# Kernel optimization log

Hardware: AMD Instinct MI355X
Metric: run time of the kernel (lower is better)

## Reference

```python
import jax, jax.numpy as jnp
import numpy as np

B, L, E, R, A = 1024, 40, 1024, 1024, 512


def setup_inputs() -> dict:
    key = jax.random.key(0)
    ks = jax.random.split(key, 20)
    s = 0.05  # weight scale to avoid gate saturation
    inp = {
        "xt": jax.random.normal(ks[0], (B, E), jnp.float32),
        "xt_mask": jnp.ones((B, 1), jnp.float32),
        "V": jax.random.normal(ks[1], (B, L, R), jnp.float32),
        "pos_feat": jax.random.normal(ks[2], (B, R), jnp.float32),
        "h1": jax.random.normal(ks[3], (1, B, R), jnp.float32),
        "c1": jax.random.normal(ks[4], (1, B, R), jnp.float32),
        "h2": jax.random.normal(ks[5], (1, B, R), jnp.float32),
        "c2": jax.random.normal(ks[6], (1, B, R), jnp.float32),
        "Wg": jax.random.normal(ks[7], (E, R), jnp.float32) * s,
        "bg": jnp.zeros((R,), jnp.float32),
        "Wi1": jax.random.normal(ks[8], (E, 4 * R), jnp.float32) * s,
        "bi1": jnp.zeros((4 * R,), jnp.float32),
        "Wa1": jax.random.normal(ks[9], (R, 4 * R), jnp.float32) * s,
        "ba1": jnp.zeros((4 * R,), jnp.float32),
        "Wh1": jax.random.normal(ks[10], (R, 4 * R), jnp.float32) * s,
        "bh1": jnp.zeros((4 * R,), jnp.float32),
        "Wi2": jax.random.normal(ks[11], (R, 4 * R), jnp.float32) * s,
        "bi2": jnp.zeros((4 * R,), jnp.float32),
        "Wa2": jax.random.normal(ks[12], (R, 4 * R), jnp.float32) * s,
        "ba2": jnp.zeros((4 * R,), jnp.float32),
        "Wh2": jax.random.normal(ks[13], (R, 4 * R), jnp.float32) * s,
        "bh2": jnp.zeros((4 * R,), jnp.float32),
        "Wv2a": jax.random.normal(ks[14], (R, A), jnp.float32) * s,
        "bv2a": jnp.zeros((A,), jnp.float32),
        "Wh2a": jax.random.normal(ks[15], (2 * R, A), jnp.float32) * s,
        "bh2a": jnp.zeros((A,), jnp.float32),
        "Wa2w": jax.random.normal(ks[16], (A, 1), jnp.float32) * s,
        "ba2w": jnp.zeros((1,), jnp.float32),
    }
    return inp


def _lstm_cell(in1, in2, h, c, Wi, bi, Wa, ba, Wh, bh, mask):
    # all_input_sums: [B, 4R]; torch gate order: i, f, o (sigmoid) then g (tanh)
    s = in1 @ Wi + bi + in2 @ Wa + ba + h @ Wh + bh
    i_g = jax.nn.sigmoid(s[:, 0 * R:1 * R])
    f_g = jax.nn.sigmoid(s[:, 1 * R:2 * R])
    o_g = jax.nn.sigmoid(s[:, 2 * R:3 * R])
    g = jnp.tanh(s[:, 3 * R:4 * R])
    c_new = f_g * c + i_g * g
    c_new = c_new * mask + c * (1.0 - mask)
    h_new = o_g * jnp.tanh(c_new)
    h_new = h_new * mask + h * (1.0 - mask)
    return h_new, c_new


def reference(xt, xt_mask, V, pos_feat, h1, c1, h2, c2,
              Wg, bg, Wi1, bi1, Wa1, ba1, Wh1, bh1,
              Wi2, bi2, Wa2, ba2, Wh2, bh2,
              Wv2a, bv2a, Wh2a, bh2a, Wa2w, ba2w):
    h1l, c1l = h1[-1], c1[-1]  # [B, R]
    h2l, c2l = h2[-1], c2[-1]
    # additive attention over L frames
    hq = jnp.concatenate([h1l, h2l], axis=1) @ Wh2a + bh2a        # [B, A]
    e = jnp.tanh(hq[:, None, :] + V @ Wv2a + bv2a) @ Wa2w + ba2w  # [B, L, 1]
    w = jax.nn.softmax(e, axis=1)                                  # softmax over L
    af = jnp.sum(w * V, axis=1)                                    # [B, R]
    # gate (dropout in eval mode -> identity)
    gate = jax.nn.relu(xt @ Wg + bg)
    gated_pos = gate * pos_feat + pos_feat
    # two-layer LSTM
    out1, c1n = _lstm_cell(xt, gated_pos, h1l, c1l, Wi1, bi1, Wa1, ba1, Wh1, bh1, xt_mask)
    out2, c2n = _lstm_cell(out1, af, h2l, c2l, Wi2, bi2, Wa2, ba2, Wh2, bh2, xt_mask)
    return (out2, out1[None], c1n[None], out2[None], c2n[None])
```

## Files before the change

kernel.cpp:

```cpp
#include <hip/hip_runtime.h>
#include <math.h>

#define BB 1024
#define LL 40
#define RR 1024

using short8 = __attribute__((ext_vector_type(8))) short;
using us8    = __attribute__((ext_vector_type(8))) unsigned short;
using f32x4  = __attribute__((ext_vector_type(4))) float;

__device__ __forceinline__ ushort f2bf(float f) {
    union { float f; unsigned u; } a; a.f = f;
    unsigned r = a.u + 0x7fffu + ((a.u >> 16) & 1u);
    return (ushort)(r >> 16);
}
__device__ __forceinline__ float bf2f(ushort u) {
    union { unsigned u; float f; } a; a.u = ((unsigned)u) << 16;
    return a.f;
}
__device__ __forceinline__ float ftanh(float x) {
    float cx = fminf(fmaxf(x, -15.f), 15.f);
    float e = __expf(2.f * cx);
    return (e - 1.f) / (e + 1.f);
}
__device__ __forceinline__ float fsigmoid(float x) {
    float cx = fminf(fmaxf(x, -30.f), 30.f);
    return 1.f / (1.f + __expf(-cx));
}

__device__ __forceinline__ void gll16(const ushort* g, ushort* l) {
    __builtin_amdgcn_global_load_lds(
        (const __attribute__((address_space(1))) void*)g,
        (__attribute__((address_space(3))) void*)l,
        16, 0, 0);
}

__global__ __launch_bounds__(256) void conv_bf16_kernel(
    const float* __restrict__ src, ushort* __restrict__ dst, int n8)
{
    const int i = blockIdx.x * 256 + threadIdx.x;
    if (i >= n8) return;
    const float4* s4 = (const float4*)(src + (size_t)i * 8);
    float4 x = s4[0], y = s4[1];
    us8 v;
    v[0] = f2bf(x.x); v[1] = f2bf(x.y); v[2] = f2bf(x.z); v[3] = f2bf(x.w);
    v[4] = f2bf(y.x); v[5] = f2bf(y.y); v[6] = f2bf(y.z); v[7] = f2bf(y.w);
    ((us8*)dst)[i] = v;
}

struct CP3 { const float* in[3]; ushort* out[3]; };
__global__ __launch_bounds__(256) void conv_bf16_batch3_kernel(CP3 p, int n8)
{
    const int z = blockIdx.y;
    const int i = blockIdx.x * 256 + threadIdx.x;
    if (i >= n8) return;
    const float4* s4 = (const float4*)(p.in[z] + (size_t)i * 8);
    float4 x = s4[0], y = s4[1];
    us8 v;
    v[0] = f2bf(x.x); v[1] = f2bf(x.y); v[2] = f2bf(x.z); v[3] = f2bf(x.w);
    v[4] = f2bf(y.x); v[5] = f2bf(y.y); v[6] = f2bf(y.z); v[7] = f2bf(y.w);
    ((us8*)p.out[z])[i] = v;
}

struct TP6 { const float* in[6]; ushort* out[6]; int N[6]; };
__global__ __launch_bounds__(256) void transpose_conv_kernel(TP6 p)
{
    const int z = blockIdx.z;
    const int Nn = p.N[z];
    const int n0 = blockIdx.x * 64;
    if (n0 >= Nn) return;
    const int k0 = blockIdx.y * 64;
    const float* in = p.in[z];
    ushort* out = p.out[z];

    __shared__ float tile[64][65];
    const int t = threadIdx.x;
    const int tx = t & 63, ty = t >> 6;
#pragma unroll
    for (int r = 0; r < 16; ++r) {
        const int row = ty * 16 + r;
        tile[row][tx] = in[(size_t)(k0 + row) * Nn + n0 + tx];
    }
    __syncthreads();
    const int n = t >> 2, kq = t & 3;
    us8 v0, v1;
#pragma unroll
    for (int j = 0; j < 8; ++j) v0[j] = f2bf(tile[kq * 16 + j][n]);
#pragma unroll
    for (int j = 0; j < 8; ++j) v1[j] = f2bf(tile[kq * 16 + 8 + j][n]);
    ushort* op = out + (size_t)(n0 + n) * 1024 + k0 + kq * 16;
    *(us8*)op = v0;
    *((us8*)op + 1) = v1;
}

template <int NP, int SK, int EPI>
__global__ __launch_bounds__(256) void gemm_gl(
    const ushort* __restrict__ A0, const ushort* __restrict__ A1, const ushort* __restrict__ A2,
    const ushort* __restrict__ W0, const ushort* __restrict__ W1, const ushort* __restrict__ W2,
    float* __restrict__ C, int M, int N,
    const float* __restrict__ hq, const float* __restrict__ bv2a,
    const float* __restrict__ Wa2w, float* __restrict__ epart)
{
    __shared__ ushort As[128 * 32];
    __shared__ ushort Bs[128 * 32];

    const int t = threadIdx.x, lane = t & 63, wave = t >> 6;
    const int wm = wave >> 1, wn = wave & 1;

    int bx, by;
    if constexpr (EPI == 2) {
        const int lin = blockIdx.y * gridDim.x + blockIdx.x;
        const int swz = (lin & 7) * 160 + (lin >> 3);
        bx = swz & 3; by = swz >> 2;
    } else { bx = blockIdx.x; by = blockIdx.y; }
    const int m0 = by * 128, n0 = bx * 128;

    const int srow = 16 * wave + (lane >> 2);
    const int skq  = lane & 3;

    f32x4 acc[4][4];
#pragma unroll
    for (int i = 0; i < 4; ++i)
#pragma unroll
        for (int j = 0; j < 4; ++j) acc[i][j] = (f32x4){0.f, 0.f, 0.f, 0.f};

    const int total = NP * 32;
    const int per   = total / SK;
    const int s0v   = blockIdx.z * per;
    const int sEnd  = s0v + per;

    for (int s = s0v; s < sEnd; ++s) {
        const int p  = (NP == 1) ? 0 : (s >> 5);
        const int k0 = (s & 31) << 5;
        const ushort* Ap = (p == 0) ? A0 : ((p == 1) ? A1 : A2);
        const ushort* Wp = (p == 0) ? W0 : ((p == 1) ? W1 : W2);
        const ushort* ga = Ap + (size_t)(m0 + srow) * 1024 + k0 + skq * 8;
        const ushort* gb = Wp + (size_t)(n0 + srow) * 1024 + k0 + skq * 8;
        gll16(ga,                 &As[512 * wave]);
        gll16(ga + 64 * 1024,     &As[2048 + 512 * wave]);
        gll16(gb,                 &Bs[512 * wave]);
        gll16(gb + 64 * 1024,     &Bs[2048 + 512 * wave]);
        __syncthreads();

        short8 aF[4], bF[4];
#pragma unroll
        for (int mi = 0; mi < 4; ++mi)
            aF[mi] = *(const short8*)&As[(wm * 64 + mi * 16 + (lane & 15)) * 32 + (lane >> 4) * 8];
#pragma unroll
        for (int ni = 0; ni < 4; ++ni)
            bF[ni] = *(const short8*)&Bs[(wn * 64 + ni * 16 + (lane & 15)) * 32 + (lane >> 4) * 8];
#pragma unroll
        for (int mi = 0; mi < 4; ++mi)
#pragma unroll
            for (int ni = 0; ni < 4; ++ni)
                acc[mi][ni] = __builtin_amdgcn_mfma_f32_16x16x32_bf16(aF[mi], bF[ni], acc[mi][ni], 0, 0, 0);
        __syncthreads();
    }

    if constexpr (EPI == 3) {
        float* Cz = C + (size_t)blockIdx.z * M * N;
#pragma unroll
        for (int ni = 0; ni < 4; ++ni) {
            const int col = n0 + wn * 64 + ni * 16 + (lane & 15);
#pragma unroll
            for (int mi = 0; mi < 4; ++mi) {
                const int row = m0 + wm * 64 + mi * 16 + ((lane >> 4) << 2);
#pragma unroll
                for (int r = 0; r < 4; ++r)
                    Cz[(size_t)(row + r) * N + col] = acc[mi][ni][r];
            }
        }
    } else if constexpr (EPI == 2) {
        float* red = (float*)As;
        float wa[4], bv[4];
        int coln[4];
#pragma unroll
        for (int ni = 0; ni < 4; ++ni) {
            coln[ni] = n0 + wn * 64 + ni * 16 + (lane & 15);
            wa[ni] = Wa2w[coln[ni]];
            bv[ni] = bv2a[coln[ni]];
        }
#pragma unroll
        for (int mi = 0; mi < 4; ++mi) {
            const int rowl = wm * 64 + mi * 16 + ((lane >> 4) << 2);
#pragma unroll
            for (int r = 0; r < 4; ++r) {
                const int row = m0 + rowl + r;
                const int b = row / LL;
                float v = 0.f;
#pragma unroll
                for (int ni = 0; ni < 4; ++ni) {
                    float x = acc[mi][ni][r] + hq[(size_t)b * 512 + coln[ni]] + bv[ni];
                    v += ftanh(x) * wa[ni];
                }
                v += __shfl_xor(v, 1);
                v += __shfl_xor(v, 2);
                v += __shfl_xor(v, 4);
                v += __shfl_xor(v, 8);
                if ((lane & 15) == 0) red[(rowl + r) * 2 + wn] = v;
            }
        }
        __syncthreads();
        if (t < 128)
            epart[(size_t)(m0 + t) * 4 + bx] = red[t * 2] + red[t * 2 + 1];
    }
}

__global__ __launch_bounds__(256) void reduce_hq_kernel(
    const float* __restrict__ part, const float* __restrict__ bias, float* __restrict__ hq)
{
    const int i = blockIdx.x * 256 + threadIdx.x;
    float s = bias[i & 511];
#pragma unroll
    for (int z = 0; z < 8; ++z) s += part[(size_t)z * 524288 + i];
    hq[i] = s;
}

__global__ __launch_bounds__(256) void reduce_gate_kernel(
    const float* __restrict__ part, const float* __restrict__ bias,
    const float* __restrict__ pos, ushort* __restrict__ gpb)
{
    const int i = blockIdx.x * 256 + threadIdx.x;
    float s = bias[i & 1023];
#pragma unroll
    for (int z = 0; z < 4; ++z) s += part[(size_t)z * 1048576 + i];
    const float g = fmaxf(s, 0.f);
    gpb[i] = f2bf(g * pos[i] + pos[i]);
}

__global__ __launch_bounds__(256) void softmax_af_kernel(
    const float* __restrict__ epart, const ushort* __restrict__ Vb,
    const float* __restrict__ ba2w, ushort* __restrict__ afb)
{
    const int b = blockIdx.x;
    const int tid = threadIdx.x;
    __shared__ float e_raw[LL];
    __shared__ float e_exp[LL];

    if (tid < LL) {
        const float* ep = &epart[(size_t)(b * LL + tid) * 4];
        float e = ba2w[0];
#pragma unroll
        for (int c = 0; c < 4; ++c) e += ep[c];
        e_raw[tid] = e;
    }
    __syncthreads();
    float mx = -1e30f;
#pragma unroll
    for (int l = 0; l < LL; ++l) mx = fmaxf(mx, e_raw[l]);
    if (tid < LL) e_exp[tid] = __expf(e_raw[tid] - mx);
    __syncthreads();
    float sum = 0.f;
#pragma unroll
    for (int l = 0; l < LL; ++l) sum += e_exp[l];
    const float inv = 1.f / sum;

    const int r4 = tid * 4;
    const ushort* vp = &Vb[(size_t)b * LL * RR + r4];
    float a0 = 0.f, a1 = 0.f, a2 = 0.f, a3 = 0.f;
#pragma unroll 8
    for (int l = 0; l < LL; ++l) {
        ushort4 v = *(const ushort4*)&vp[(size_t)l * RR];
        const float w = e_exp[l];
        a0 += w * bf2f(v.x); a1 += w * bf2f(v.y);
        a2 += w * bf2f(v.z); a3 += w * bf2f(v.w);
    }
    ushort* op = &afb[(size_t)b * RR + r4];
    op[0] = f2bf(a0 * inv); op[1] = f2bf(a1 * inv);
    op[2] = f2bf(a2 * inv); op[3] = f2bf(a3 * inv);
}

__global__ __launch_bounds__(256) void lstm_finish4_kernel(
    const float* __restrict__ part,
    const float* __restrict__ bi, const float* __restrict__ ba, const float* __restrict__ bh,
    const float* __restrict__ c_in, const float* __restrict__ h_in, const float* __restrict__ mask,
    float* __restrict__ h_out, float* __restrict__ h_out2,
    float* __restrict__ c_out, ushort* __restrict__ h_bf)
{
    const int i = blockIdx.x * 256 + threadIdx.x;
    const int b = i >> 10;
    const int r = i & 1023;
    float sg[4];
#pragma unroll
    for (int g = 0; g < 4; ++g) {
        const int gr = g * 1024 + r;
        float s = bi[gr] + ba[gr] + bh[gr];
#pragma unroll
        for (int z = 0; z < 4; ++z)
            s += part[(size_t)z * 4194304 + (size_t)b * 4096 + gr];
        sg[g] = s;
    }
    const float ig = fsigmoid(sg[0]);
    const float fg = fsigmoid(sg[1]);
    const float og = fsigmoid(sg[2]);
    const float gt = ftanh(sg[3]);
    const float m = mask[b];
    const float c = c_in[i];
    float cn = fg * c + ig * gt;
    cn = cn * m + c * (1.f - m);
    const float h = h_in[i];
    float hn = og * ftanh(cn);
    hn = hn * m + h * (1.f - m);
    h_out[i] = hn;
    if (h_out2) h_out2[i] = hn;
    c_out[i] = cn;
    if (h_bf) h_bf[i] = f2bf(hn);
}

extern "C" void kernel_launch(void* const* d_in, const int* in_sizes, int n_in,
                              void* d_out, int out_size, void* d_ws, size_t ws_size,
                              hipStream_t stream) {
    const float* xt   = (const float*)d_in[0];
    const float* mask = (const float*)d_in[1];
    const float* V    = (const float*)d_in[2];
    const float* pos  = (const float*)d_in[3];
    const float* h1   = (const float*)d_in[4];
    const float* c1   = (const float*)d_in[5];
    const float* h2   = (const float*)d_in[6];
    const float* c2   = (const float*)d_in[7];
    const float* Wg   = (const float*)d_in[8];
    const float* bg   = (const float*)d_in[9];
    const float* Wi1  = (const float*)d_in[10];
    const float* bi1  = (const float*)d_in[11];
    const float* Wa1  = (const float*)d_in[12];
    const float* ba1  = (const float*)d_in[13];
    const float* Wh1  = (const float*)d_in[14];
    const float* bh1  = (const float*)d_in[15];
    const float* Wi2  = (const float*)d_in[16];
    const float* bi2  = (const float*)d_in[17];
    const float* Wa2  = (const float*)d_in[18];
    const float* ba2  = (const float*)d_in[19];
    const float* Wh2  = (const float*)d_in[20];
    const float* bh2  = (const float*)d_in[21];
    const float* Wv2a = (const float*)d_in[22];
    const float* bv2a = (const float*)d_in[23];
    const float* Wh2a = (const float*)d_in[24];
    const float* bh2a = (const float*)d_in[25];
    const float* Wa2w = (const float*)d_in[26];
    const float* ba2w = (const float*)d_in[27];

    float* out = (float*)d_out;
    float* out2  = out;
    float* out1  = out + (size_t)BB * RR;
    float* c1n   = out + 2 * (size_t)BB * RR;
    float* out2b = out + 3 * (size_t)BB * RR;
    float* c2n   = out + 4 * (size_t)BB * RR;

    ushort* wsu = (ushort*)d_ws;
    size_t o = 0;
    ushort* Vb     = wsu + o; o += (size_t)40960 * 1024;
    ushort* Wh2aT0 = wsu + o; o += (size_t)512 * 1024;
    ushort* Wh2aT1 = wsu + o; o += (size_t)512 * 1024;
    ushort* WgT    = wsu + o; o += (size_t)1024 * 1024;
    ushort* Wv2aT  = wsu + o; o += (size_t)512 * 1024;
    ushort* Wi1T   = wsu + o; o += (size_t)4096 * 1024;
    ushort* Wa1T   = wsu + o; o += (size_t)4096 * 1024;
    ushort* Wh1T   = wsu + o; o += (size_t)4096 * 1024;
    ushort* Wi2T   = wsu + o; o += (size_t)4096 * 1024;
    ushort* Wa2T   = wsu + o; o += (size_t)4096 * 1024;
    ushort* Wh2T   = wsu + o; o += (size_t)4096 * 1024;
    ushort* xtb    = wsu + o; o += (size_t)1024 * 1024;
    ushort* h1b    = wsu + o; o += (size_t)1024 * 1024;
    ushort* h2b    = wsu + o; o += (size_t)1024 * 1024;
    ushort* gpb    = wsu + o; o += (size_t)1024 * 1024;
    ushort* afb    = wsu + o; o += (size_t)1024 * 1024;
    ushort* out1b  = wsu + o; o += (size_t)1024 * 1024;
    float* wsf    = (float*)(wsu + o);
    float* hqf    = wsf;
    float* epart  = hqf + 524288;
    float* partSm = epart + 163840;
    float* partK  = (float*)Vb;

    const dim3 blk(256);

    conv_bf16_kernel<<<dim3(20480), blk, 0, stream>>>(V, Vb, 5242880);
    {
        CP3 p; p.in[0] = xt; p.in[1] = h1; p.in[2] = h2;
        p.out[0] = xtb; p.out[1] = h1b; p.out[2] = h2b;
        conv_bf16_batch3_kernel<<<dim3(512, 3), blk, 0, stream>>>(p, 131072);
    }
    {
        TP6 p;
        p.in[0] = Wi1; p.in[1] = Wa1; p.in[2] = Wh1;
        p.in[3] = Wi2; p.in[4] = Wa2; p.in[5] = Wh2;
        p.out[0] = Wi1T; p.out[1] = Wa1T; p.out[2] = Wh1T;
        p.out[3] = Wi2T; p.out[4] = Wa2T; p.out[5] = Wh2T;
        for (int z = 0; z < 6; ++z) p.N[z] = 4096;
        transpose_conv_kernel<<<dim3(64, 16, 6), blk, 0, stream>>>(p);
    }
    {
        TP6 p;
        p.in[0] = Wh2a; p.in[1] = Wh2a + (size_t)1024 * 512;
        p.in[2] = Wg;   p.in[3] = Wv2a;
        p.out[0] = Wh2aT0; p.out[1] = Wh2aT1; p.out[2] = WgT; p.out[3] = Wv2aT;
        p.N[0] = 512; p.N[1] = 512; p.N[2] = 1024; p.N[3] = 512;
        p.in[4] = nullptr; p.in[5] = nullptr; p.out[4] = nullptr; p.out[5] = nullptr;
        p.N[4] = 0; p.N[5] = 0;
        transpose_conv_kernel<<<dim3(16, 16, 4), blk, 0, stream>>>(p);
    }

    gemm_gl<2, 8, 3><<<dim3(4, 8, 8), blk, 0, stream>>>(
        h1b, h2b, nullptr, Wh2aT0, Wh2aT1, nullptr,
        partSm, 1024, 512, nullptr, nullptr, nullptr, nullptr);
    reduce_hq_kernel<<<dim3(2048), blk, 0, stream>>>(partSm, bh2a, hqf);

    gemm_gl<1, 4, 3><<<dim3(8, 8, 4), blk, 0, stream>>>(
        xtb, nullptr, nullptr, WgT, nullptr, nullptr,
        partSm, 1024, 1024, nullptr, nullptr, nullptr, nullptr);
    reduce_gate_kernel<<<dim3(4096), blk, 0, stream>>>(partSm, bg, pos, gpb);

    gemm_gl<1, 1, 2><<<dim3(4, 320, 1), blk, 0, stream>>>(
        Vb, nullptr, nullptr, Wv2aT, nullptr, nullptr,
        nullptr, 40960, 512, hqf, bv2a, Wa2w, epart);
    softmax_af_kernel<<<dim3(BB), blk, 0, stream>>>(epart, Vb, ba2w, afb);

    gemm_gl<3, 4, 3><<<dim3(32, 8, 4), blk, 0, stream>>>(
        xtb, gpb, h1b, Wi1T, Wa1T, Wh1T,
        partK, 1024, 4096, nullptr, nullptr, nullptr, nullptr);
    lstm_finish4_kernel<<<dim3(4096), blk, 0, stream>>>(
        partK, bi1, ba1, bh1, c1, h1, mask, out1, nullptr, c1n, out1b);

    gemm_gl<3, 4, 3><<<dim3(32, 8, 4), blk, 0, stream>>>(
        out1b, afb, h2b, Wi2T, Wa2T, Wh2T,
        partK, 1024, 4096, nullptr, nullptr, nullptr, nullptr);
    lstm_finish4_kernel<<<dim3(4096), blk, 0, stream>>>(
        partK, bi2, ba2, bh2, c2, h2, mask, out2, out2b, c2n, nullptr);
}
```

Baseline: 329.0 us.

## Replace GEMM with 256x256 double-buffered 512-thread kernel and bf16 split-K partials

```diff
diff --git a/kernel.cpp b/kernel.cpp
--- a/kernel.cpp
+++ b/kernel.cpp
@@ -93,96 +93,144 @@
     *((us8*)op + 1) = v1;
 }
 
-template <int NP, int SK, int EPI>
-__global__ __launch_bounds__(256) void gemm_gl(
+template <int NP, int NTZ, int EPI>
+__global__ __launch_bounds__(512) void gemm256(
     const ushort* __restrict__ A0, const ushort* __restrict__ A1, const ushort* __restrict__ A2,
     const ushort* __restrict__ W0, const ushort* __restrict__ W1, const ushort* __restrict__ W2,
-    float* __restrict__ C, int M, int N,
+    ushort* __restrict__ Cp, int M, int N,
     const float* __restrict__ hq, const float* __restrict__ bv2a,
     const float* __restrict__ Wa2w, float* __restrict__ epart)
 {
-    __shared__ ushort As[128 * 32];
-    __shared__ ushort Bs[128 * 32];
-
-    const int t = threadIdx.x, lane = t & 63, wave = t >> 6;
-    const int wm = wave >> 1, wn = wave & 1;
-
-    int bx, by;
+    __shared__ ushort As[2][256 * 64];
+    __shared__ ushort Bs[2][256 * 64];
+
+    const int t = threadIdx.x, l = t & 63, w = t >> 6;
+    const int wm = w >> 2, wn = w & 3;
+
+    int mblk, nblk, bz;
     if constexpr (EPI == 2) {
-        const int lin = blockIdx.y * gridDim.x + blockIdx.x;
-        const int swz = (lin & 7) * 160 + (lin >> 3);
-        bx = swz & 3; by = swz >> 2;
-    } else { bx = blockIdx.x; by = blockIdx.y; }
-    const int m0 = by * 128, n0 = bx * 128;
-
-    const int srow = 16 * wave + (lane >> 2);
-    const int skq  = lane & 3;
-
-    f32x4 acc[4][4];
-#pragma unroll
-    for (int i = 0; i < 4; ++i)
+        const int lin = blockIdx.x;
+        const int swz = (lin & 7) * 40 + (lin >> 3);
+        nblk = swz & 1; mblk = swz >> 1; bz = 0;
+    } else {
+        const int Dx = gridDim.x, Dy = gridDim.y;
+        const int lin = blockIdx.x + blockIdx.y * Dx + blockIdx.z * Dx * gridDim.y;
+        const int nwg = Dx * Dy * gridDim.z;
+        const int cpx = nwg >> 3;
+        const int swz = (lin & 7) * cpx + (lin >> 3);
+        mblk = swz % Dx;
+        const int rest = swz / Dx;
+        nblk = rest % Dy;
+        bz = rest / Dy;
+    }
+    const int m0 = mblk * 256, n0 = nblk * 256;
+
+    f32x4 acc[8][4];
+#pragma unroll
+    for (int i = 0; i < 8; ++i)
 #pragma unroll
         for (int j = 0; j < 4; ++j) acc[i][j] = (f32x4){0.f, 0.f, 0.f, 0.f};
 
-    const int total = NP * 32;
-    const int per   = total / SK;
-    const int s0v   = blockIdx.z * per;
-    const int sEnd  = s0v + per;
-
-    for (int s = s0v; s < sEnd; ++s) {
-        const int p  = (NP == 1) ? 0 : (s >> 5);
-        const int k0 = (s & 31) << 5;
+    const int rsub = w * 8 + (l >> 3);
+    const int csw  = ((l & 7) ^ (l >> 3)) * 8;
+
+    const int kx0 = ((0 * 4 + (l >> 4)) ^ (l & 7)) * 8;
+    const int kx1 = ((1 * 4 + (l >> 4)) ^ (l & 7)) * 8;
+
+    const int gt0 = bz * NTZ;
+
+    auto stage = [&](int s, int buf) {
+        const int p  = (NP == 1) ? 0 : (s >> 4);
+        const int k0 = (s & 15) << 6;
         const ushort* Ap = (p == 0) ? A0 : ((p == 1) ? A1 : A2);
         const ushort* Wp = (p == 0) ? W0 : ((p == 1) ? W1 : W2);
-        const ushort* ga = Ap + (size_t)(m0 + srow) * 1024 + k0 + skq * 8;
-        const ushort* gb = Wp + (size_t)(n0 + srow) * 1024 + k0 + skq * 8;
-        gll16(ga,                 &As[512 * wave]);
-        gll16(ga + 64 * 1024,     &As[2048 + 512 * wave]);
-        gll16(gb,                 &Bs[512 * wave]);
-        gll16(gb + 64 * 1024,     &Bs[2048 + 512 * wave]);
-        __syncthreads();
-
-        short8 aF[4], bF[4];
-#pragma unroll
-        for (int mi = 0; mi < 4; ++mi)
-            aF[mi] = *(const short8*)&As[(wm * 64 + mi * 16 + (lane & 15)) * 32 + (lane >> 4) * 8];
-#pragma unroll
-        for (int ni = 0; ni < 4; ++ni)
-            bF[ni] = *(const short8*)&Bs[(wn * 64 + ni * 16 + (lane & 15)) * 32 + (lane >> 4) * 8];
-#pragma unroll
-        for (int mi = 0; mi < 4; ++mi)
-#pragma unroll
-            for (int ni = 0; ni < 4; ++ni)
-                acc[mi][ni] = __builtin_amdgcn_mfma_f32_16x16x32_bf16(aF[mi], bF[ni], acc[mi][ni], 0, 0, 0);
-        __syncthreads();
+#pragma unroll
+        for (int j = 0; j < 4; ++j) {
+            gll16(Ap + (size_t)(m0 + j * 64 + rsub) * 1024 + k0 + csw,
+                  &As[buf][(j * 64 + w * 8) * 64]);
+            gll16(Wp + (size_t)(n0 + j * 64 + rsub) * 1024 + k0 + csw,
+                  &Bs[buf][(j * 64 + w * 8) * 64]);
+        }
+    };
+
+    stage(gt0, 0);
+    stage(gt0 + 1, 1);
+    asm volatile("s_waitcnt vmcnt(8)" ::: "memory");
+    __builtin_amdgcn_s_barrier();
+    asm volatile("" ::: "memory");
+
+    int cur = 0;
+    for (int ti = 0; ti < NTZ; ++ti) {
+#pragma unroll
+        for (int qm = 0; qm < 2; ++qm) {
+            short8 aF[4][2];
+#pragma unroll
+            for (int mi = 0; mi < 4; ++mi) {
+                const int ro = (wm * 128 + (qm * 4 + mi) * 16 + (l & 15)) * 64;
+                aF[mi][0] = *(const short8*)&As[cur][ro + kx0];
+                aF[mi][1] = *(const short8*)&As[cur][ro + kx1];
+            }
+#pragma unroll
+            for (int qn = 0; qn < 2; ++qn) {
+                short8 bF[2][2];
+#pragma unroll
+                for (int ni = 0; ni < 2; ++ni) {
+                    const int ro = (wn * 64 + (qn * 2 + ni) * 16 + (l & 15)) * 64;
+                    bF[ni][0] = *(const short8*)&Bs[cur][ro + kx0];
+                    bF[ni][1] = *(const short8*)&Bs[cur][ro + kx1];
+                }
+                __builtin_amdgcn_s_setprio(1);
+#pragma unroll
+                for (int mi = 0; mi < 4; ++mi)
+#pragma unroll
+                    for (int ni = 0; ni < 2; ++ni) {
+                        acc[qm * 4 + mi][qn * 2 + ni] = __builtin_amdgcn_mfma_f32_16x16x32_bf16(
+                            aF[mi][0], bF[ni][0], acc[qm * 4 + mi][qn * 2 + ni], 0, 0, 0);
+                        acc[qm * 4 + mi][qn * 2 + ni] = __builtin_amdgcn_mfma_f32_16x16x32_bf16(
+                            aF[mi][1], bF[ni][1], acc[qm * 4 + mi][qn * 2 + ni], 0, 0, 0);
+                    }
+                __builtin_amdgcn_s_setprio(0);
+            }
+        }
+        asm volatile("" ::: "memory");
+        __builtin_amdgcn_s_barrier();
+        asm volatile("" ::: "memory");
+        if (ti + 2 < NTZ) stage(gt0 + ti + 2, cur);
+        if (ti + 1 < NTZ) {
+            if (ti + 2 < NTZ) asm volatile("s_waitcnt vmcnt(8)" ::: "memory");
+            else              asm volatile("s_waitcnt vmcnt(0)" ::: "memory");
+            __builtin_amdgcn_s_barrier();
+            asm volatile("" ::: "memory");
+        }
+        cur ^= 1;
     }
 
     if constexpr (EPI == 3) {
-        float* Cz = C + (size_t)blockIdx.z * M * N;
+        ushort* Cz = Cp + (size_t)bz * M * N;
 #pragma unroll
         for (int ni = 0; ni < 4; ++ni) {
-            const int col = n0 + wn * 64 + ni * 16 + (lane & 15);
-#pragma unroll
-            for (int mi = 0; mi < 4; ++mi) {
-                const int row = m0 + wm * 64 + mi * 16 + ((lane >> 4) << 2);
+            const int col = n0 + wn * 64 + ni * 16 + (l & 15);
+#pragma unroll
+            for (int mi = 0; mi < 8; ++mi) {
+                const int row = m0 + wm * 128 + mi * 16 + ((l >> 4) << 2);
 #pragma unroll
                 for (int r = 0; r < 4; ++r)
-                    Cz[(size_t)(row + r) * N + col] = acc[mi][ni][r];
+                    Cz[(size_t)(row + r) * N + col] = f2bf(acc[mi][ni][r]);
             }
         }
     } else if constexpr (EPI == 2) {
-        float* red = (float*)As;
+        float* red = (float*)&As[0][0];
         float wa[4], bv[4];
         int coln[4];
 #pragma unroll
         for (int ni = 0; ni < 4; ++ni) {
-            coln[ni] = n0 + wn * 64 + ni * 16 + (lane & 15);
+            coln[ni] = n0 + wn * 64 + ni * 16 + (l & 15);
             wa[ni] = Wa2w[coln[ni]];
             bv[ni] = bv2a[coln[ni]];
         }
 #pragma unroll
-        for (int mi = 0; mi < 4; ++mi) {
-            const int rowl = wm * 64 + mi * 16 + ((lane >> 4) << 2);
+        for (int mi = 0; mi < 8; ++mi) {
+            const int rowl = wm * 128 + mi * 16 + ((l >> 4) << 2);
 #pragma unroll
             for (int r = 0; r < 4; ++r) {
                 const int row = m0 + rowl + r;
@@ -197,33 +245,35 @@
                 v += __shfl_xor(v, 2);
                 v += __shfl_xor(v, 4);
                 v += __shfl_xor(v, 8);
-                if ((lane & 15) == 0) red[(rowl + r) * 2 + wn] = v;
+                if ((l & 15) == 0) red[(rowl + r) * 4 + wn] = v;
             }
         }
         __syncthreads();
-        if (t < 128)
-            epart[(size_t)(m0 + t) * 4 + bx] = red[t * 2] + red[t * 2 + 1];
-    }
-}
-
-__global__ __launch_bounds__(256) void reduce_hq_kernel(
-    const float* __restrict__ part, const float* __restrict__ bias, float* __restrict__ hq)
+        if (t < 256) {
+            float s = red[t * 4] + red[t * 4 + 1] + red[t * 4 + 2] + red[t * 4 + 3];
+            epart[(size_t)(m0 + t) * 2 + nblk] = s;
+        }
+    }
+}
+
+__global__ __launch_bounds__(256) void reduce_hq_b_kernel(
+    const ushort* __restrict__ part, const float* __restrict__ bias, float* __restrict__ hq)
 {
     const int i = blockIdx.x * 256 + threadIdx.x;
     float s = bias[i & 511];
 #pragma unroll
-    for (int z = 0; z < 8; ++z) s += part[(size_t)z * 524288 + i];
+    for (int z = 0; z < 8; ++z) s += bf2f(part[(size_t)z * 524288 + i]);
     hq[i] = s;
 }
 
-__global__ __launch_bounds__(256) void reduce_gate_kernel(
-    const float* __restrict__ part, const float* __restrict__ bias,
+__global__ __launch_bounds__(256) void reduce_gate_b_kernel(
+    const ushort* __restrict__ part, const float* __restrict__ bias,
     const float* __restrict__ pos, ushort* __restrict__ gpb)
 {
     const int i = blockIdx.x * 256 + threadIdx.x;
     float s = bias[i & 1023];
 #pragma unroll
-    for (int z = 0; z < 4; ++z) s += part[(size_t)z * 1048576 + i];
+    for (int z = 0; z < 4; ++z) s += bf2f(part[(size_t)z * 1048576 + i]);
     const float g = fmaxf(s, 0.f);
     gpb[i] = f2bf(g * pos[i] + pos[i]);
 }
@@ -238,40 +288,37 @@
     __shared__ float e_exp[LL];
 
     if (tid < LL) {
-        const float* ep = &epart[(size_t)(b * LL + tid) * 4];
-        float e = ba2w[0];
-#pragma unroll
-        for (int c = 0; c < 4; ++c) e += ep[c];
-        e_raw[tid] = e;
+        const float* ep = &epart[(size_t)(b * LL + tid) * 2];
+        e_raw[tid] = ba2w[0] + ep[0] + ep[1];
     }
     __syncthreads();
     float mx = -1e30f;
 #pragma unroll
-    for (int l = 0; l < LL; ++l) mx = fmaxf(mx, e_raw[l]);
+    for (int ll = 0; ll < LL; ++ll) mx = fmaxf(mx, e_raw[ll]);
     if (tid < LL) e_exp[tid] = __expf(e_raw[tid] - mx);
     __syncthreads();
     float sum = 0.f;
 #pragma unroll
-    for (int l = 0; l < LL; ++l) sum += e_exp[l];
+    for (int ll = 0; ll < LL; ++ll) sum += e_exp[ll];
     const float inv = 1.f / sum;
 
     const int r4 = tid * 4;
     const ushort* vp = &Vb[(size_t)b * LL * RR + r4];
     float a0 = 0.f, a1 = 0.f, a2 = 0.f, a3 = 0.f;
 #pragma unroll 8
-    for (int l = 0; l < LL; ++l) {
-        ushort4 v = *(const ushort4*)&vp[(size_t)l * RR];
-        const float w = e_exp[l];
-        a0 += w * bf2f(v.x); a1 += w * bf2f(v.y);
-        a2 += w * bf2f(v.z); a3 += w * bf2f(v.w);
+    for (int ll = 0; ll < LL; ++ll) {
+        ushort4 v = *(const ushort4*)&vp[(size_t)ll * RR];
+        const float wgt = e_exp[ll];
+        a0 += wgt * bf2f(v.x); a1 += wgt * bf2f(v.y);
+        a2 += wgt * bf2f(v.z); a3 += wgt * bf2f(v.w);
     }
     ushort* op = &afb[(size_t)b * RR + r4];
     op[0] = f2bf(a0 * inv); op[1] = f2bf(a1 * inv);
     op[2] = f2bf(a2 * inv); op[3] = f2bf(a3 * inv);
 }
 
-__global__ __launch_bounds__(256) void lstm_finish4_kernel(
-    const float* __restrict__ part,
+__global__ __launch_bounds__(256) void lstm_finishb_kernel(
+    const ushort* __restrict__ part,
     const float* __restrict__ bi, const float* __restrict__ ba, const float* __restrict__ bh,
     const float* __restrict__ c_in, const float* __restrict__ h_in, const float* __restrict__ mask,
     float* __restrict__ h_out, float* __restrict__ h_out2,
@@ -287,7 +334,7 @@
         float s = bi[gr] + ba[gr] + bh[gr];
 #pragma unroll
         for (int z = 0; z < 4; ++z)
-            s += part[(size_t)z * 4194304 + (size_t)b * 4096 + gr];
+            s += bf2f(part[(size_t)z * 4194304 + (size_t)b * 4096 + gr]);
         sg[g] = s;
     }
     const float ig = fsigmoid(sg[0]);
@@ -365,13 +412,14 @@
     ushort* gpb    = wsu + o; o += (size_t)1024 * 1024;
     ushort* afb    = wsu + o; o += (size_t)1024 * 1024;
     ushort* out1b  = wsu + o; o += (size_t)1024 * 1024;
+    ushort* partSb = wsu + o; o += (size_t)8 * 1024 * 512;
     float* wsf    = (float*)(wsu + o);
     float* hqf    = wsf;
     float* epart  = hqf + 524288;
-    float* partSm = epart + 163840;
-    float* partK  = (float*)Vb;
+    ushort* partKb = Vb;
 
     const dim3 blk(256);
+    const dim3 blk5(512);
 
     conv_bf16_kernel<<<dim3(20480), blk, 0, stream>>>(V, Vb, 5242880);
     {
@@ -399,30 +447,30 @@
         transpose_conv_kernel<<<dim3(16, 16, 4), blk, 0, stream>>>(p);
     }
 
-    gemm_gl<2, 8, 3><<<dim3(4, 8, 8), blk, 0, stream>>>(
+    gemm256<2, 4, 3><<<dim3(4, 2, 8), blk5, 0, stream>>>(
         h1b, h2b, nullptr, Wh2aT0, Wh2aT1, nullptr,
-        partSm, 1024, 512, nullptr, nullptr, nullptr, nullptr);
-    reduce_hq_kernel<<<dim3(2048), blk, 0, stream>>>(partSm, bh2a, hqf);
-
-    gemm_gl<1, 4, 3><<<dim3(8, 8, 4), blk, 0, stream>>>(
+        partSb, 1024, 512, nullptr, nullptr, nullptr, nullptr);
+    reduce_hq_b_kernel<<<dim3(2048), blk, 0, stream>>>(partSb, bh2a, hqf);
+
+    gemm256<1, 4, 3><<<dim3(4, 4, 4), blk5, 0, stream>>>(
         xtb, nullptr, nullptr, WgT, nullptr, nullptr,
-        partSm, 1024, 1024, nullptr, nullptr, nullptr, nullptr);
-    reduce_gate_kernel<<<dim3(4096), blk, 0, stream>>>(partSm, bg, pos, gpb);
-
-    gemm_gl<1, 1, 2><<<dim3(4, 320, 1), blk, 0, stream>>>(
+        partSb, 1024, 1024, nullptr, nullptr, nullptr, nullptr);
+    reduce_gate_b_kernel<<<dim3(4096), blk, 0, stream>>>(partSb, bg, pos, gpb);
+
+    gemm256<1, 16, 2><<<dim3(320), blk5, 0, stream>>>(
         Vb, nullptr, nullptr, Wv2aT, nullptr, nullptr,
         nullptr, 40960, 512, hqf, bv2a, Wa2w, epart);
     softmax_af_kernel<<<dim3(BB), blk, 0, stream>>>(epart, Vb, ba2w, afb);
 
-    gemm_gl<3, 4, 3><<<dim3(32, 8, 4), blk, 0, stream>>>(
+    gemm256<3, 12, 3><<<dim3(4, 16, 4), blk5, 0, stream>>>(
         xtb, gpb, h1b, Wi1T, Wa1T, Wh1T,
-        partK, 1024, 4096, nullptr, nullptr, nullptr, nullptr);
-    lstm_finish4_kernel<<<dim3(4096), blk, 0, stream>>>(
-        partK, bi1, ba1, bh1, c1, h1, mask, out1, nullptr, c1n, out1b);
-
-    gemm_gl<3, 4, 3><<<dim3(32, 8, 4), blk, 0, stream>>>(
+        partKb, 1024, 4096, nullptr, nullptr, nullptr, nullptr);
+    lstm_finishb_kernel<<<dim3(4096), blk, 0, stream>>>(
+        partKb, bi1, ba1, bh1, c1, h1, mask, out1, nullptr, c1n, out1b);
+
+    gemm256<3, 12, 3><<<dim3(4, 16, 4), blk5, 0, stream>>>(
         out1b, afb, h2b, Wi2T, Wa2T, Wh2T,
-        partK, 1024, 4096, nullptr, nullptr, nullptr, nullptr);
-    lstm_finish4_kernel<<<dim3(4096), blk, 0, stream>>>(
-        partK, bi2, ba2, bh2, c2, h2, mask, out2, out2b, c2n, nullptr);
-}
+        partKb, 1024, 4096, nullptr, nullptr, nullptr, nullptr);
+    lstm_finishb_kernel<<<dim3(4096), blk, 0, stream>>>(
+        partKb, bi2, ba2, bh2, c2, h2, mask, out2, out2b, c2n, nullptr);
+}
```

Measured after the change: 383.0 us. 16.4% more time.

## Double GEMM K-tile to 64 with XOR-swizzled LDS and bf16 split-K partials

Applied to the files above, without the earlier changes.

```diff
diff --git a/kernel.cpp b/kernel.cpp
--- a/kernel.cpp
+++ b/kernel.cpp
@@ -97,15 +97,15 @@
 __global__ __launch_bounds__(256) void gemm_gl(
     const ushort* __restrict__ A0, const ushort* __restrict__ A1, const ushort* __restrict__ A2,
     const ushort* __restrict__ W0, const ushort* __restrict__ W1, const ushort* __restrict__ W2,
-    float* __restrict__ C, int M, int N,
+    ushort* __restrict__ Cp, int M, int N,
     const float* __restrict__ hq, const float* __restrict__ bv2a,
     const float* __restrict__ Wa2w, float* __restrict__ epart)
 {
-    __shared__ ushort As[128 * 32];
-    __shared__ ushort Bs[128 * 32];
-
-    const int t = threadIdx.x, lane = t & 63, wave = t >> 6;
-    const int wm = wave >> 1, wn = wave & 1;
+    __shared__ ushort As[128 * 64];
+    __shared__ ushort Bs[128 * 64];
+
+    const int t = threadIdx.x, l = t & 63, w = t >> 6;
+    const int wm = w >> 1, wn = w & 1;
 
     int bx, by;
     if constexpr (EPI == 2) {
@@ -115,8 +115,11 @@
     } else { bx = blockIdx.x; by = blockIdx.y; }
     const int m0 = by * 128, n0 = bx * 128;
 
-    const int srow = 16 * wave + (lane >> 2);
-    const int skq  = lane & 3;
+    const int srow = l >> 3;
+    const int csw  = ((l & 7) ^ (l >> 3)) * 8;
+
+    const int kx0 = ((0 + (l >> 4)) ^ (l & 7)) * 8;
+    const int kx1 = ((4 + (l >> 4)) ^ (l & 7)) * 8;
 
     f32x4 acc[4][4];
 #pragma unroll
@@ -124,50 +127,60 @@
 #pragma unroll
         for (int j = 0; j < 4; ++j) acc[i][j] = (f32x4){0.f, 0.f, 0.f, 0.f};
 
-    const int total = NP * 32;
+    const int total = NP * 16;
     const int per   = total / SK;
     const int s0v   = blockIdx.z * per;
     const int sEnd  = s0v + per;
 
     for (int s = s0v; s < sEnd; ++s) {
-        const int p  = (NP == 1) ? 0 : (s >> 5);
-        const int k0 = (s & 31) << 5;
+        const int p  = (NP == 1) ? 0 : (s >> 4);
+        const int k0 = (s & 15) << 6;
         const ushort* Ap = (p == 0) ? A0 : ((p == 1) ? A1 : A2);
         const ushort* Wp = (p == 0) ? W0 : ((p == 1) ? W1 : W2);
-        const ushort* ga = Ap + (size_t)(m0 + srow) * 1024 + k0 + skq * 8;
-        const ushort* gb = Wp + (size_t)(n0 + srow) * 1024 + k0 + skq * 8;
-        gll16(ga,                 &As[512 * wave]);
-        gll16(ga + 64 * 1024,     &As[2048 + 512 * wave]);
-        gll16(gb,                 &Bs[512 * wave]);
-        gll16(gb + 64 * 1024,     &Bs[2048 + 512 * wave]);
+#pragma unroll
+        for (int j = 0; j < 4; ++j) {
+            const int rb = w * 32 + j * 8;
+            gll16(Ap + (size_t)(m0 + rb + srow) * 1024 + k0 + csw, &As[rb * 64]);
+            gll16(Wp + (size_t)(n0 + rb + srow) * 1024 + k0 + csw, &Bs[rb * 64]);
+        }
         __syncthreads();
 
-        short8 aF[4], bF[4];
+        short8 aF[4][2], bF[4][2];
+#pragma unroll
+        for (int mi = 0; mi < 4; ++mi) {
+            const int ro = (wm * 64 + mi * 16 + (l & 15)) * 64;
+            aF[mi][0] = *(const short8*)&As[ro + kx0];
+            aF[mi][1] = *(const short8*)&As[ro + kx1];
+        }
+#pragma unroll
+        for (int ni = 0; ni < 4; ++ni) {
+            const int ro = (wn * 64 + ni * 16 + (l & 15)) * 64;
+            bF[ni][0] = *(const short8*)&Bs[ro + kx0];
+            bF[ni][1] = *(const short8*)&Bs[ro + kx1];
+        }
 #pragma unroll
         for (int mi = 0; mi < 4; ++mi)
-            aF[mi] = *(const short8*)&As[(wm * 64 + mi * 16 + (lane & 15)) * 32 + (lane >> 4) * 8];
-#pragma unroll
-        for (int ni = 0; ni < 4; ++ni)
-            bF[ni] = *(const short8*)&Bs[(wn * 64 + ni * 16 + (lane & 15)) * 32 + (lane >> 4) * 8];
-#pragma unroll
-        for (int mi = 0; mi < 4; ++mi)
-#pragma unroll
-            for (int ni = 0; ni < 4; ++ni)
-                acc[mi][ni] = __builtin_amdgcn_mfma_f32_16x16x32_bf16(aF[mi], bF[ni], acc[mi][ni], 0, 0, 0);
+#pragma unroll
+            for (int ni = 0; ni < 4; ++ni) {
+                acc[mi][ni] = __builtin_amdgcn_mfma_f32_16x16x32_bf16(
+                    aF[mi][0], bF[ni][0], acc[mi][ni], 0, 0, 0);
+                acc[mi][ni] = __builtin_amdgcn_mfma_f32_16x16x32_bf16(
+                    aF[mi][1], bF[ni][1], acc[mi][ni], 0, 0, 0);
+            }
         __syncthreads();
     }
 
     if constexpr (EPI == 3) {
-        float* Cz = C + (size_t)blockIdx.z * M * N;
+        ushort* Cz = Cp + (size_t)blockIdx.z * M * N;
 #pragma unroll
         for (int ni = 0; ni < 4; ++ni) {
-            const int col = n0 + wn * 64 + ni * 16 + (lane & 15);
+            const int col = n0 + wn * 64 + ni * 16 + (l & 15);
 #pragma unroll
             for (int mi = 0; mi < 4; ++mi) {
-                const int row = m0 + wm * 64 + mi * 16 + ((lane >> 4) << 2);
+                const int row = m0 + wm * 64 + mi * 16 + ((l >> 4) << 2);
 #pragma unroll
                 for (int r = 0; r < 4; ++r)
-                    Cz[(size_t)(row + r) * N + col] = acc[mi][ni][r];
+                    Cz[(size_t)(row + r) * N + col] = f2bf(acc[mi][ni][r]);
             }
         }
     } else if constexpr (EPI == 2) {
@@ -176,13 +189,13 @@
         int coln[4];
 #pragma unroll
         for (int ni = 0; ni < 4; ++ni) {
-            coln[ni] = n0 + wn * 64 + ni * 16 + (lane & 15);
+            coln[ni] = n0 + wn * 64 + ni * 16 + (l & 15);
             wa[ni] = Wa2w[coln[ni]];
             bv[ni] = bv2a[coln[ni]];
         }
 #pragma unroll
         for (int mi = 0; mi < 4; ++mi) {
-            const int rowl = wm * 64 + mi * 16 + ((lane >> 4) << 2);
+            const int rowl = wm * 64 + mi * 16 + ((l >> 4) << 2);
 #pragma unroll
             for (int r = 0; r < 4; ++r) {
                 const int row = m0 + rowl + r;
@@ -197,7 +210,7 @@
                 v += __shfl_xor(v, 2);
                 v += __shfl_xor(v, 4);
                 v += __shfl_xor(v, 8);
-                if ((lane & 15) == 0) red[(rowl + r) * 2 + wn] = v;
+                if ((l & 15) == 0) red[(rowl + r) * 2 + wn] = v;
             }
         }
         __syncthreads();
@@ -206,24 +219,24 @@
     }
 }
 
-__global__ __launch_bounds__(256) void reduce_hq_kernel(
-    const float* __restrict__ part, const float* __restrict__ bias, float* __restrict__ hq)
+__global__ __launch_bounds__(256) void reduce_hq_b_kernel(
+    const ushort* __restrict__ part, const float* __restrict__ bias, float* __restrict__ hq)
 {
     const int i = blockIdx.x * 256 + threadIdx.x;
     float s = bias[i & 511];
 #pragma unroll
-    for (int z = 0; z < 8; ++z) s += part[(size_t)z * 524288 + i];
+    for (int z = 0; z < 8; ++z) s += bf2f(part[(size_t)z * 524288 + i]);
     hq[i] = s;
 }
 
-__global__ __launch_bounds__(256) void reduce_gate_kernel(
-    const float* __restrict__ part, const float* __restrict__ bias,
+__global__ __launch_bounds__(256) void reduce_gate_b_kernel(
+    const ushort* __restrict__ part, const float* __restrict__ bias,
     const float* __restrict__ pos, ushort* __restrict__ gpb)
 {
     const int i = blockIdx.x * 256 + threadIdx.x;
     float s = bias[i & 1023];
 #pragma unroll
-    for (int z = 0; z < 4; ++z) s += part[(size_t)z * 1048576 + i];
+    for (int z = 0; z < 4; ++z) s += bf2f(part[(size_t)z * 1048576 + i]);
     const float g = fmaxf(s, 0.f);
     gpb[i] = f2bf(g * pos[i] + pos[i]);
 }
@@ -247,31 +260,31 @@
     __syncthreads();
     float mx = -1e30f;
 #pragma unroll
-    for (int l = 0; l < LL; ++l) mx = fmaxf(mx, e_raw[l]);
+    for (int ll = 0; ll < LL; ++ll) mx = fmaxf(mx, e_raw[ll]);
     if (tid < LL) e_exp[tid] = __expf(e_raw[tid] - mx);
     __syncthreads();
     float sum = 0.f;
 #pragma unroll
-    for (int l = 0; l < LL; ++l) sum += e_exp[l];
+    for (int ll = 0; ll < LL; ++ll) sum += e_exp[ll];
     const float inv = 1.f / sum;
 
     const int r4 = tid * 4;
     const ushort* vp = &Vb[(size_t)b * LL * RR + r4];
     float a0 = 0.f, a1 = 0.f, a2 = 0.f, a3 = 0.f;
 #pragma unroll 8
-    for (int l = 0; l < LL; ++l) {
-        ushort4 v = *(const ushort4*)&vp[(size_t)l * RR];
-        const float w = e_exp[l];
-        a0 += w * bf2f(v.x); a1 += w * bf2f(v.y);
-        a2 += w * bf2f(v.z); a3 += w * bf2f(v.w);
+    for (int ll = 0; ll < LL; ++ll) {
+        ushort4 v = *(const ushort4*)&vp[(size_t)ll * RR];
+        const float wgt = e_exp[ll];
+        a0 += wgt * bf2f(v.x); a1 += wgt * bf2f(v.y);
+        a2 += wgt * bf2f(v.z); a3 += wgt * bf2f(v.w);
     }
     ushort* op = &afb[(size_t)b * RR + r4];
     op[0] = f2bf(a0 * inv); op[1] = f2bf(a1 * inv);
     op[2] = f2bf(a2 * inv); op[3] = f2bf(a3 * inv);
 }
 
-__global__ __launch_bounds__(256) void lstm_finish4_kernel(
-    const float* __restrict__ part,
+__global__ __launch_bounds__(256) void lstm_finishb_kernel(
+    const ushort* __restrict__ part,
     const float* __restrict__ bi, const float* __restrict__ ba, const float* __restrict__ bh,
     const float* __restrict__ c_in, const float* __restrict__ h_in, const float* __restrict__ mask,
     float* __restrict__ h_out, float* __restrict__ h_out2,
@@ -287,7 +300,7 @@
         float s = bi[gr] + ba[gr] + bh[gr];
 #pragma unroll
         for (int z = 0; z < 4; ++z)
-            s += part[(size_t)z * 4194304 + (size_t)b * 4096 + gr];
+            s += bf2f(part[(size_t)z * 4194304 + (size_t)b * 4096 + gr]);
         sg[g] = s;
     }
     const float ig = fsigmoid(sg[0]);
@@ -365,11 +378,11 @@
     ushort* gpb    = wsu + o; o += (size_t)1024 * 1024;
     ushort* afb    = wsu + o; o += (size_t)1024 * 1024;
     ushort* out1b  = wsu + o; o += (size_t)1024 * 1024;
+    ushort* partSb = wsu + o; o += (size_t)8 * 1024 * 512;
     float* wsf    = (float*)(wsu + o);
     float* hqf    = wsf;
     float* epart  = hqf + 524288;
-    float* partSm = epart + 163840;
-    float* partK  = (float*)Vb;
+    ushort* partKb = Vb;
 
     const dim3 blk(256);
 
@@ -401,13 +414,13 @@
 
     gemm_gl<2, 8, 3><<<dim3(4, 8, 8), blk, 0, stream>>>(
         h1b, h2b, nullptr, Wh2aT0, Wh2aT1, nullptr,
-        partSm, 1024, 512, nullptr, nullptr, nullptr, nullptr);
-    reduce_hq_kernel<<<dim3(2048), blk, 0, stream>>>(partSm, bh2a, hqf);
+        partSb, 1024, 512, nullptr, nullptr, nullptr, nullptr);
+    reduce_hq_b_kernel<<<dim3(2048), blk, 0, stream>>>(partSb, bh2a, hqf);
 
     gemm_gl<1, 4, 3><<<dim3(8, 8, 4), blk, 0, stream>>>(
         xtb, nullptr, nullptr, WgT, nullptr, nullptr,
-        partSm, 1024, 1024, nullptr, nullptr, nullptr, nullptr);
-    reduce_gate_kernel<<<dim3(4096), blk, 0, stream>>>(partSm, bg, pos, gpb);
+        partSb, 1024, 1024, nullptr, nullptr, nullptr, nullptr);
+    reduce_gate_b_kernel<<<dim3(4096), blk, 0, stream>>>(partSb, bg, pos, gpb);
 
     gemm_gl<1, 1, 2><<<dim3(4, 320, 1), blk, 0, stream>>>(
         Vb, nullptr, nullptr, Wv2aT, nullptr, nullptr,
@@ -416,13 +429,13 @@
 
     gemm_gl<3, 4, 3><<<dim3(32, 8, 4), blk, 0, stream>>>(
         xtb, gpb, h1b, Wi1T, Wa1T, Wh1T,
-        partK, 1024, 4096, nullptr, nullptr, nullptr, nullptr);
-    lstm_finish4_kernel<<<dim3(4096), blk, 0, stream>>>(
-        partK, bi1, ba1, bh1, c1, h1, mask, out1, nullptr, c1n, out1b);
+        partKb, 1024, 4096, nullptr, nullptr, nullptr, nullptr);
+    lstm_finishb_kernel<<<dim3(4096), blk, 0, stream>>>(
+        partKb, bi1, ba1, bh1, c1, h1, mask, out1, nullptr, c1n, out1b);
 
     gemm_gl<3, 4, 3><<<dim3(32, 8, 4), blk, 0, stream>>>(
         out1b, afb, h2b, Wi2T, Wa2T, Wh2T,
-        partK, 1024, 4096, nullptr, nullptr, nullptr, nullptr);
-    lstm_finish4_kernel<<<dim3(4096), blk, 0, stream>>>(
-        partK, bi2, ba2, bh2, c2, h2, mask, out2, out2b, c2n, nullptr);
-}
+        partKb, 1024, 4096, nullptr, nullptr, nullptr, nullptr);
+    lstm_finishb_kernel<<<dim3(4096), blk, 0, stream>>>(
+        partKb, bi2, ba2, bh2, c2, h2, mask, out2, out2b, c2n, nullptr);
+}
```

New measurement: 322.1 us. 2.1% less time.
